# Kernel optimization log

Measured on AMD Instinct MI355X. Metric: run time of the kernel, lower is better.

The kernel has to match this reference:

```python
import jax, jax.numpy as jnp
import numpy as np

N = 100000          # num nodes
E = 3200000         # num edges (avg degree 32)
C = 64              # num_classes
L = 10000           # num labeled nodes
NUM_LAYERS = 10
ALPHA = 0.9


def setup_inputs() -> dict:
    key = jax.random.key(0)
    k1, k2, k3, k4 = jax.random.split(key, 4)
    y_soft = jax.random.normal(k1, (N, C), dtype=jnp.float32)
    y_true = jax.random.randint(k2, (L,), 0, C)
    mask = jax.random.randint(k3, (L,), 0, N)
    edge_index = jax.random.randint(k4, (2, E), 0, N)
    return {"y_soft": y_soft, "y_true": y_true, "mask": mask,
            "edge_index": edge_index}


def reference(y_soft, y_true, mask, edge_index):
    row, col = edge_index[0], edge_index[1]  # source -> target

    # smooth(): normalize predictions, then clamp labeled nodes to one-hot y
    z = jax.nn.softmax(y_soft, axis=1)                       # [N, C]
    y_onehot = jax.nn.one_hot(y_true, C, dtype=z.dtype)      # [L, C]
    z = z.at[mask].set(y_onehot)

    # gcn_norm without self-loops: w_e = deg^-1/2[row] * deg^-1/2[col]
    ones = jnp.ones((edge_index.shape[1],), dtype=z.dtype)
    deg = jax.ops.segment_sum(ones, col, num_segments=N)     # [N]
    dinv = jnp.where(deg > 0,
                     jax.lax.rsqrt(jnp.maximum(deg, 1e-12)),
                     jnp.zeros_like(deg))
    norm = dinv[row] * dinv[col]                             # [E]

    # Label spreading: Z <- clip(alpha * (D^-1/2 A D^-1/2) Z + (1-alpha) Z0, 0, 1)
    res = (1.0 - ALPHA) * z
    out = z
    for _ in range(NUM_LAYERS):
        msg = norm[:, None] * out[row]                       # [E, C] gather
        agg = jax.ops.segment_sum(msg, col, num_segments=N)  # [N, C] scatter-add
        out = jnp.clip(ALPHA * agg + res, 0.0, 1.0)          # PyG post_step clamp
    return out
```

## Files before the change

### kernel.cpp

```cpp
#include <hip/hip_runtime.h>
#include <hip/hip_fp16.h>

#define NCLS 64
#define ALPHA 0.9f
#define SCAN_BS 256
#define SCAN_CHUNK 1024
#define NBUCK 256
#define BSHIFT 9
#define BSPAN 512
#define P1_CAP 3200
#define ROWMASK 0x7FFFFFu

__device__ __forceinline__ float wave_max64(float v) {
    #pragma unroll
    for (int o = 32; o > 0; o >>= 1) v = fmaxf(v, __shfl_xor(v, o, 64));
    return v;
}
__device__ __forceinline__ float wave_sum64(float v) {
    #pragma unroll
    for (int o = 32; o > 0; o >>= 1) v += __shfl_xor(v, o, 64);
    return v;
}

__global__ void winner_k(const int* __restrict__ mask, int* __restrict__ winner, int L) {
    int i = blockIdx.x * blockDim.x + threadIdx.x;
    if (i < L) atomicMax(&winner[mask[i]], i);
}

__global__ void bcount_k(const int* __restrict__ col, int* __restrict__ bcnt, int E) {
    __shared__ int h[NBUCK];
    int t = threadIdx.x;
    h[t] = 0;
    __syncthreads();
    int stride = gridDim.x * blockDim.x;
    for (int e = blockIdx.x * blockDim.x + t; e < E; e += stride)
        atomicAdd(&h[col[e] >> BSHIFT], 1);
    __syncthreads();
    if (h[t]) atomicAdd(&bcnt[t], h[t]);
}

__global__ void bscan_k(const int* __restrict__ bcnt, int* __restrict__ bbase,
                        int* __restrict__ bcur, int E) {
    __shared__ int lds[NBUCK];
    int t = threadIdx.x;
    int v = bcnt[t];
    lds[t] = v;
    __syncthreads();
    for (int o = 1; o < NBUCK; o <<= 1) {
        int x = (t >= o) ? lds[t - o] : 0;
        __syncthreads();
        lds[t] += x;
        __syncthreads();
    }
    int ex = lds[t] - v;
    bbase[t] = ex;
    bcur[t] = ex;
    if (t == NBUCK - 1) bbase[NBUCK] = E;
}

__global__ void binpass1_k(const int* __restrict__ row, const int* __restrict__ col,
                           int* __restrict__ bcur, unsigned* __restrict__ bpk,
                           int E, int chunk) {
    __shared__ int hist[NBUCK];
    __shared__ int scn[NBUCK];
    __shared__ int lbase[NBUCK];
    __shared__ int lcur[NBUCK];
    __shared__ unsigned pay[P1_CAP];
    __shared__ unsigned char bkt[P1_CAP];
    int t = threadIdx.x;
    int e0 = blockIdx.x * chunk;
    int e1 = min(e0 + chunk, E);
    if (e0 >= E) return;
    hist[t] = 0;
    __syncthreads();
    for (int e = e0 + t; e < e1; e += 256)
        atomicAdd(&hist[col[e] >> BSHIFT], 1);
    __syncthreads();
    scn[t] = hist[t];
    __syncthreads();
    for (int o = 1; o < 256; o <<= 1) {
        int y = (t >= o) ? scn[t - o] : 0;
        __syncthreads();
        scn[t] += y;
        __syncthreads();
    }
    int cnt = hist[t];
    int lstart = scn[t] - cnt;
    int gb = 0;
    if (cnt > 0) gb = atomicAdd(&bcur[t], cnt);
    lbase[t] = gb - lstart;
    lcur[t] = lstart;
    __syncthreads();
    for (int e = e0 + t; e < e1; e += 256) {
        int c = col[e];
        int b = c >> BSHIFT;
        int p = atomicAdd(&lcur[b], 1);
        pay[p] = ((unsigned)(c & (BSPAN - 1)) << 23) | (unsigned)row[e];
        bkt[p] = (unsigned char)b;
    }
    __syncthreads();
    int n = e1 - e0;
    for (int i = t; i < n; i += 256) {
        unsigned w = pay[i];
        int b = bkt[i];
        bpk[lbase[b] + i] = w;
    }
}

__global__ void bdeg_k(const int* __restrict__ bbase, const unsigned* __restrict__ bpk,
                       int* __restrict__ deg, float* __restrict__ dinv, int Nn) {
    __shared__ int hist[BSPAN];
    int b = blockIdx.x;
    int nb0 = b * BSPAN;
    if (nb0 >= Nn) return;
    int t = threadIdx.x;
    hist[t] = 0;
    hist[t + 256] = 0;
    __syncthreads();
    int e0 = bbase[b];
    int e1 = bbase[b + 1];
    for (int e = e0 + t; e < e1; e += 256)
        atomicAdd(&hist[bpk[e] >> 23], 1);
    __syncthreads();
    int n0 = nb0 + t;
    if (n0 < Nn) {
        int d = hist[t];
        deg[n0] = d;
        dinv[n0] = (d > 0) ? rsqrtf((float)d) : 0.0f;
    }
    int n1 = nb0 + 256 + t;
    if (n1 < Nn) {
        int d = hist[t + 256];
        deg[n1] = d;
        dinv[n1] = (d > 0) ? rsqrtf((float)d) : 0.0f;
    }
}

__global__ void scan_local_k(const int* __restrict__ deg, int* __restrict__ rowptr,
                             int* __restrict__ bsum, int n) {
    __shared__ int lds[SCAN_BS];
    int base = blockIdx.x * SCAN_CHUNK;
    int t = threadIdx.x;
    int v[4];
    int s = 0;
    #pragma unroll
    for (int k = 0; k < 4; ++k) {
        int i = base + t * 4 + k;
        v[k] = (i < n) ? deg[i] : 0;
        s += v[k];
    }
    lds[t] = s;
    __syncthreads();
    for (int o = 1; o < SCAN_BS; o <<= 1) {
        int x = (t >= o) ? lds[t - o] : 0;
        __syncthreads();
        lds[t] += x;
        __syncthreads();
    }
    int ex = (t > 0) ? lds[t - 1] : 0;
    #pragma unroll
    for (int k = 0; k < 4; ++k) {
        int i = base + t * 4 + k;
        if (i < n) rowptr[i] = ex;
        ex += v[k];
    }
    if (t == SCAN_BS - 1) bsum[blockIdx.x] = lds[t];
}

__global__ void scan_bsum_k(int* __restrict__ bsum, int nb) {
    __shared__ int lds[SCAN_BS];
    int t = threadIdx.x;
    int v = (t < nb) ? bsum[t] : 0;
    lds[t] = v;
    __syncthreads();
    for (int o = 1; o < SCAN_BS; o <<= 1) {
        int x = (t >= o) ? lds[t - o] : 0;
        __syncthreads();
        lds[t] += x;
        __syncthreads();
    }
    if (t < nb) bsum[t] = lds[t] - v;
}

__global__ void scan_add_k(int* __restrict__ rowptr, const int* __restrict__ bsum, int n) {
    int i = blockIdx.x * blockDim.x + threadIdx.x;
    if (i < n) rowptr[i] += bsum[i / SCAN_CHUNK];
}

__global__ void binpass2_k(const int* __restrict__ rowptr, const unsigned* __restrict__ bpk,
                           int* __restrict__ src, int Nn, int E) {
    __shared__ int cur[BSPAN];
    int b = blockIdx.x;
    int nb0 = b * BSPAN;
    if (nb0 >= Nn) return;
    int nb1 = min(nb0 + BSPAN, Nn);
    int t = threadIdx.x;
    for (int i = nb0 + t; i < nb1; i += 256) cur[i - nb0] = rowptr[i];
    __syncthreads();
    int e0 = rowptr[nb0];
    int e1 = (nb1 < Nn) ? rowptr[nb1] : E;
    for (int e = e0 + t; e < e1; e += 256) {
        unsigned w = bpk[e];
        int p = atomicAdd(&cur[w >> 23], 1);
        src[p] = (int)(w & ROWMASK);
    }
}

__global__ void init_k(const float* __restrict__ y, const int* __restrict__ winner,
                       const int* __restrict__ ytrue, const float* __restrict__ dinv,
                       __half* __restrict__ res_h, __half* __restrict__ vh, int Nn) {
    int lane = threadIdx.x & 63;
    int wave = (blockIdx.x * blockDim.x + threadIdx.x) >> 6;
    int nwaves = (gridDim.x * blockDim.x) >> 6;
    for (int n = wave; n < Nn; n += nwaves) {
        float v = y[(size_t)n * NCLS + lane];
        float m = wave_max64(v);
        float e = expf(v - m);
        float s = wave_sum64(e);
        float u = e / s;
        int w = winner[n];
        if (w >= 0) u = (lane == ytrue[w]) ? 1.0f : 0.0f;
        res_h[(size_t)n * NCLS + lane] = __float2half((1.0f - ALPHA) * u);
        vh[(size_t)n * NCLS + lane] = __float2half(dinv[n] * u);
    }
}

#define GATHER(dst, s) do {                                                      \
    float2 f_ = __half22float2(vin2[(size_t)(s) * 32 + k]);                      \
    dst.x += f_.x; dst.y += f_.y;                                                \
} while (0)

__global__ void pull_k(const int* __restrict__ rowptr, const int* __restrict__ deg,
                       const int* __restrict__ src, const float* __restrict__ dinv,
                       const __half2* __restrict__ vin2, const __half2* __restrict__ res2,
                       __half2* __restrict__ vout2, float2* __restrict__ uout2,
                       int n_nodes, int last) {
    int lane = threadIdx.x & 63;
    int half_id = lane >> 5;
    int k = lane & 31;
    int n = (blockIdx.x * blockDim.x + threadIdx.x) >> 6;
    if (n >= n_nodes) return;
    int start = rowptr[n];
    int len = deg[n];
    float2 a0 = make_float2(0.f, 0.f), a1 = make_float2(0.f, 0.f);
    float2 a2 = make_float2(0.f, 0.f), a3 = make_float2(0.f, 0.f);
    float2 a4 = make_float2(0.f, 0.f), a5 = make_float2(0.f, 0.f);
    float2 a6 = make_float2(0.f, 0.f), a7 = make_float2(0.f, 0.f);
    for (int base = 0; base < len; base += 64) {
        int m = min(64, len - base);
        int sv = (lane < m) ? __builtin_nontemporal_load(&src[start + base + lane]) : 0;
        int j = 0;
        for (; j + 16 <= m; j += 16) {
            int s0 = __shfl(sv, j      + half_id, 64);
            int s1 = __shfl(sv, j + 2  + half_id, 64);
            int s2 = __shfl(sv, j + 4  + half_id, 64);
            int s3 = __shfl(sv, j + 6  + half_id, 64);
            int s4 = __shfl(sv, j + 8  + half_id, 64);
            int s5 = __shfl(sv, j + 10 + half_id, 64);
            int s6 = __shfl(sv, j + 12 + half_id, 64);
            int s7 = __shfl(sv, j + 14 + half_id, 64);
            GATHER(a0, s0); GATHER(a1, s1); GATHER(a2, s2); GATHER(a3, s3);
            GATHER(a4, s4); GATHER(a5, s5); GATHER(a6, s6); GATHER(a7, s7);
        }
        for (; j + 2 <= m; j += 2) {
            int s0 = __shfl(sv, j + half_id, 64);
            GATHER(a0, s0);
        }
        if (j < m) {
            int s0 = __shfl(sv, j, 64);
            if (half_id == 0) GATHER(a0, s0);
        }
    }
    float sx = ((a0.x + a1.x) + (a2.x + a3.x)) + ((a4.x + a5.x) + (a6.x + a7.x));
    float sy = ((a0.y + a1.y) + (a2.y + a3.y)) + ((a4.y + a5.y) + (a6.y + a7.y));
    sx += __shfl_xor(sx, 32, 64);
    sy += __shfl_xor(sy, 32, 64);
    float di = dinv[n];
    unsigned rraw = __builtin_nontemporal_load(
        reinterpret_cast<const unsigned*>(&res2[(size_t)n * 32 + k]));
    union { unsigned u; __half2 h; } cv; cv.u = rraw;
    float2 r = __half22float2(cv.h);
    float u0 = fminf(fmaxf(ALPHA * (di * sx) + r.x, 0.0f), 1.0f);
    float u1 = fminf(fmaxf(ALPHA * (di * sy) + r.y, 0.0f), 1.0f);
    if (lane < 32) {
        size_t idx = (size_t)n * 32 + k;
        if (last) {
            union { float2 f; unsigned long long b; } cf; cf.f = make_float2(u0, u1);
            __builtin_nontemporal_store(cf.b, reinterpret_cast<unsigned long long*>(&uout2[idx]));
        } else {
            __half2 hv = __floats2half2_rn(di * u0, di * u1);
            union { __half2 h; unsigned b; } ch; ch.h = hv;
            __builtin_nontemporal_store(ch.b, reinterpret_cast<unsigned*>(&vout2[idx]));
        }
    }
}

extern "C" void kernel_launch(void* const* d_in, const int* in_sizes, int n_in,
                              void* d_out, int out_size, void* d_ws, size_t ws_size,
                              hipStream_t stream) {
    const float* y_soft = (const float*)d_in[0];
    const int* y_true  = (const int*)d_in[1];
    const int* mask    = (const int*)d_in[2];
    const int* edge    = (const int*)d_in[3];

    const int NC = in_sizes[0];
    const int Nn = NC / NCLS;
    const int L  = in_sizes[1];
    const int E  = in_sizes[3] / 2;

    const int* row = edge;
    const int* col = edge + E;

    float2* uout2 = (float2*)d_out;

    char* ws = (char*)d_ws;
    size_t off = 0;
    auto alloc = [&](size_t bytes) { char* p = ws + off; off += (bytes + 255) & ~(size_t)255; return p; };
    size_t reg0 = (size_t)E * 4;
    size_t vh_bytes = (size_t)NC * 2;
    if (2 * vh_bytes > reg0) reg0 = 2 * vh_bytes;
    char* region0 = alloc(reg0);
    unsigned* bpk = (unsigned*)region0;
    __half* vhA   = (__half*)region0;
    __half* vhB   = (__half*)(region0 + vh_bytes);
    __half* res_h = (__half*)alloc((size_t)NC * 2);
    int*   src    = (int*)alloc((size_t)E * 4);
    int*   deg    = (int*)alloc((size_t)Nn * 4);
    int*   rowptr = (int*)alloc((size_t)Nn * 4);
    float* dinv   = (float*)alloc((size_t)Nn * 4);
    int*   winner = (int*)alloc((size_t)Nn * 4);
    int*   bcnt   = (int*)alloc((size_t)NBUCK * 4);
    int*   bbase  = (int*)alloc((size_t)(NBUCK + 1) * 4);
    int*   bcur   = (int*)alloc((size_t)NBUCK * 4);
    int*   bsum   = (int*)alloc((size_t)SCAN_BS * 4);

    const int NB = (Nn + SCAN_CHUNK - 1) / SCAN_CHUNK;
    const int NBK = (Nn + BSPAN - 1) / BSPAN;

    hipMemsetAsync(winner, 0xFF, (size_t)Nn * 4, stream);
    hipMemsetAsync(bcnt, 0, (size_t)NBUCK * 4, stream);

    winner_k<<<(L + 255) / 256, 256, 0, stream>>>(mask, winner, L);

    bcount_k<<<1024, 256, 0, stream>>>(col, bcnt, E);
    bscan_k<<<1, NBUCK, 0, stream>>>(bcnt, bbase, bcur, E);
    const int chunk = P1_CAP;
    const int nchunks = (E + chunk - 1) / chunk;
    binpass1_k<<<nchunks, 256, 0, stream>>>(row, col, bcur, bpk, E, chunk);
    bdeg_k<<<NBK, 256, 0, stream>>>(bbase, bpk, deg, dinv, Nn);
    scan_local_k<<<NB, SCAN_BS, 0, stream>>>(deg, rowptr, bsum, Nn);
    scan_bsum_k<<<1, SCAN_BS, 0, stream>>>(bsum, NB);
    scan_add_k<<<(Nn + 255) / 256, 256, 0, stream>>>(rowptr, bsum, Nn);
    binpass2_k<<<NBK, 256, 0, stream>>>(rowptr, bpk, src, Nn, E);

    init_k<<<2048, 256, 0, stream>>>(y_soft, winner, y_true, dinv, res_h, vhA, Nn);

    const int pull_blocks = (Nn * NCLS + 255) / 256;
    for (int it = 0; it < 10; ++it) {
        const __half2* vin2 = (const __half2*)((it & 1) ? vhB : vhA);
        __half2* vout2      = (__half2*)((it & 1) ? vhA : vhB);
        pull_k<<<pull_blocks, 256, 0, stream>>>(rowptr, deg, src, dinv,
                                                vin2, (const __half2*)res_h,
                                                vout2, uout2, Nn, it == 9);
    }
}
```

Measured before the change: 894.5 us.

## Split class dimension into four slices for cache-local feature gathers

Feature storage is changed from node-major [N,64] fp16 to four slices of 16 classes each ([4][N][16]). Each pull wave now handles one node's slice, with 8 lanes per edge covering 32 bytes and 8 edges gathered per instruction. Slice-major scheduling means concurrently running waves touch only a 3.2MB slice, which should keep gathers in L2/MALL. The cost is four times as many waves, each re-reading the row pointers and edge indices, plus narrower 32-byte random accesses.

```diff
diff --git a/kernel.cpp b/kernel.cpp
--- a/kernel.cpp
+++ b/kernel.cpp
@@ -2,6 +2,7 @@
 #include <hip/hip_fp16.h>
 
 #define NCLS 64
+#define NSLICE 4
 #define ALPHA 0.9f
 #define SCAN_BS 256
 #define SCAN_CHUNK 1024
@@ -220,13 +221,14 @@
         float u = e / s;
         int w = winner[n];
         if (w >= 0) u = (lane == ytrue[w]) ? 1.0f : 0.0f;
-        res_h[(size_t)n * NCLS + lane] = __float2half((1.0f - ALPHA) * u);
-        vh[(size_t)n * NCLS + lane] = __float2half(dinv[n] * u);
+        size_t idx = ((size_t)(lane >> 4) * Nn + n) * 16 + (lane & 15);
+        res_h[idx] = __float2half((1.0f - ALPHA) * u);
+        vh[idx] = __float2half(dinv[n] * u);
     }
 }
 
 #define GATHER(dst, s) do {                                                      \
-    float2 f_ = __half22float2(vin2[(size_t)(s) * 32 + k]);                      \
+    float2 f_ = __half22float2(vslice[(size_t)(s) * 8 + c]);                     \
     dst.x += f_.x; dst.y += f_.y;                                                \
 } while (0)
 
@@ -234,63 +236,63 @@
                        const int* __restrict__ src, const float* __restrict__ dinv,
                        const __half2* __restrict__ vin2, const __half2* __restrict__ res2,
                        __half2* __restrict__ vout2, float2* __restrict__ uout2,
-                       int n_nodes, int last) {
+                       int Nn, int last) {
     int lane = threadIdx.x & 63;
-    int half_id = lane >> 5;
-    int k = lane & 31;
-    int n = (blockIdx.x * blockDim.x + threadIdx.x) >> 6;
-    if (n >= n_nodes) return;
+    int subgrp = lane >> 3;
+    int c = lane & 7;
+    int w = (blockIdx.x * blockDim.x + threadIdx.x) >> 6;
+    int cb = w / Nn;
+    int n = w - cb * Nn;
+    if (cb >= NSLICE) return;
+    const __half2* vslice = vin2 + (size_t)cb * Nn * 8;
     int start = rowptr[n];
     int len = deg[n];
     float2 a0 = make_float2(0.f, 0.f), a1 = make_float2(0.f, 0.f);
     float2 a2 = make_float2(0.f, 0.f), a3 = make_float2(0.f, 0.f);
-    float2 a4 = make_float2(0.f, 0.f), a5 = make_float2(0.f, 0.f);
-    float2 a6 = make_float2(0.f, 0.f), a7 = make_float2(0.f, 0.f);
     for (int base = 0; base < len; base += 64) {
         int m = min(64, len - base);
         int sv = (lane < m) ? __builtin_nontemporal_load(&src[start + base + lane]) : 0;
         int j = 0;
-        for (; j + 16 <= m; j += 16) {
-            int s0 = __shfl(sv, j      + half_id, 64);
-            int s1 = __shfl(sv, j + 2  + half_id, 64);
-            int s2 = __shfl(sv, j + 4  + half_id, 64);
-            int s3 = __shfl(sv, j + 6  + half_id, 64);
-            int s4 = __shfl(sv, j + 8  + half_id, 64);
-            int s5 = __shfl(sv, j + 10 + half_id, 64);
-            int s6 = __shfl(sv, j + 12 + half_id, 64);
-            int s7 = __shfl(sv, j + 14 + half_id, 64);
+        for (; j + 32 <= m; j += 32) {
+            int s0 = __shfl(sv, j      + subgrp, 64);
+            int s1 = __shfl(sv, j + 8  + subgrp, 64);
+            int s2 = __shfl(sv, j + 16 + subgrp, 64);
+            int s3 = __shfl(sv, j + 24 + subgrp, 64);
             GATHER(a0, s0); GATHER(a1, s1); GATHER(a2, s2); GATHER(a3, s3);
-            GATHER(a4, s4); GATHER(a5, s5); GATHER(a6, s6); GATHER(a7, s7);
         }
-        for (; j + 2 <= m; j += 2) {
-            int s0 = __shfl(sv, j + half_id, 64);
+        for (; j + 8 <= m; j += 8) {
+            int s0 = __shfl(sv, j + subgrp, 64);
             GATHER(a0, s0);
         }
         if (j < m) {
-            int s0 = __shfl(sv, j, 64);
-            if (half_id == 0) GATHER(a0, s0);
+            int s0 = __shfl(sv, j + subgrp, 64);
+            if (j + subgrp < m) GATHER(a0, s0);
         }
     }
-    float sx = ((a0.x + a1.x) + (a2.x + a3.x)) + ((a4.x + a5.x) + (a6.x + a7.x));
-    float sy = ((a0.y + a1.y) + (a2.y + a3.y)) + ((a4.y + a5.y) + (a6.y + a7.y));
-    sx += __shfl_xor(sx, 32, 64);
-    sy += __shfl_xor(sy, 32, 64);
+    float sx = (a0.x + a1.x) + (a2.x + a3.x);
+    float sy = (a0.y + a1.y) + (a2.y + a3.y);
+    #pragma unroll
+    for (int mask = 8; mask <= 32; mask <<= 1) {
+        sx += __shfl_xor(sx, mask, 64);
+        sy += __shfl_xor(sy, mask, 64);
+    }
     float di = dinv[n];
+    size_t ridx = ((size_t)cb * Nn + n) * 8 + c;
     unsigned rraw = __builtin_nontemporal_load(
-        reinterpret_cast<const unsigned*>(&res2[(size_t)n * 32 + k]));
+        reinterpret_cast<const unsigned*>(&res2[ridx]));
     union { unsigned u; __half2 h; } cv; cv.u = rraw;
     float2 r = __half22float2(cv.h);
     float u0 = fminf(fmaxf(ALPHA * (di * sx) + r.x, 0.0f), 1.0f);
     float u1 = fminf(fmaxf(ALPHA * (di * sy) + r.y, 0.0f), 1.0f);
-    if (lane < 32) {
-        size_t idx = (size_t)n * 32 + k;
+    if (subgrp == 0) {
         if (last) {
             union { float2 f; unsigned long long b; } cf; cf.f = make_float2(u0, u1);
-            __builtin_nontemporal_store(cf.b, reinterpret_cast<unsigned long long*>(&uout2[idx]));
+            __builtin_nontemporal_store(cf.b,
+                reinterpret_cast<unsigned long long*>(&uout2[(size_t)n * 32 + cb * 8 + c]));
         } else {
             __half2 hv = __floats2half2_rn(di * u0, di * u1);
             union { __half2 h; unsigned b; } ch; ch.h = hv;
-            __builtin_nontemporal_store(ch.b, reinterpret_cast<unsigned*>(&vout2[idx]));
+            __builtin_nontemporal_store(ch.b, reinterpret_cast<unsigned*>(&vout2[ridx]));
         }
     }
 }
@@ -355,7 +357,8 @@
 
     init_k<<<2048, 256, 0, stream>>>(y_soft, winner, y_true, dinv, res_h, vhA, Nn);
 
-    const int pull_blocks = (Nn * NCLS + 255) / 256;
+    const long long total_waves = (long long)NSLICE * Nn;
+    const int pull_blocks = (int)((total_waves * 64 + 255) / 256);
     for (int it = 0; it < 10; ++it) {
         const __half2* vin2 = (const __half2*)((it & 1) ? vhB : vhA);
         __half2* vout2      = (__half2*)((it & 1) ? vhA : vhB);
```

Measured after the change: 1.985 ms. 2.22x slower.
